# Kernel tuning notes

Measured on AMD Instinct MI355X. Metric: run time of the kernel, lower is better.

Reference implementation:

```python
import jax, jax.numpy as jnp
import numpy as np

# Decoder (keras) config: embed_dim=128, num_heads=8, num_att_layers=3, clip=10.0
B, NQ, NC, E, H, L, D = 512, 64, 1000, 128, 8, 3, 4
HD = E // H          # head_depth = 16
CLIP = 10.0


def setup_inputs() -> dict:
    key = jax.random.key(0)
    ks = jax.random.split(key, 12)
    s = 1.0 / np.sqrt(E)

    def w(k, shape):
        return jax.random.normal(k, shape, jnp.float32) * s

    return {
        "h": jax.random.normal(ks[0], (B, NQ, E), jnp.float32),
        "c": jax.random.normal(ks[1], (B, NC, E), jnp.float32),
        "mask": jnp.zeros((B, NQ, NC + 1), bool),
        "clusters": jnp.zeros((B, D, NC), bool),
        "depot_id": 0,
        # stacked per-layer GAT (multi-head self-attention) params [L, E, E]/[L, E]
        "gat_Wq": w(ks[2], (L, E, E)), "gat_bq": jnp.zeros((L, E), jnp.float32),
        "gat_Wk": w(ks[3], (L, E, E)), "gat_bk": jnp.zeros((L, E), jnp.float32),
        "gat_Wv": w(ks[4], (L, E, E)), "gat_bv": jnp.zeros((L, E), jnp.float32),
        "gat_Wo": w(ks[5], (L, E, E)), "gat_bo": jnp.zeros((L, E), jnp.float32),
        # decoder query/key dense layers (use_bias=True)
        "Wq": w(ks[6], (E, E)), "bq": jnp.zeros((E,), jnp.float32),
        "Wk": w(ks[7], (E, E)), "bk": jnp.zeros((E,), jnp.float32),
    }


def _mha_layer(x, Wq, bq, Wk, bk, Wv, bv, Wo, bo):
    # One Graph_Attention_Module: multi-head self-attention + residual.
    Bx, N, Ex = x.shape
    q = (x @ Wq + bq).reshape(Bx, N, H, HD)
    k = (x @ Wk + bk).reshape(Bx, N, H, HD)
    v = (x @ Wv + bv).reshape(Bx, N, H, HD)
    att = jax.nn.softmax(jnp.einsum('bqhd,bkhd->bhqk', q, k) / np.sqrt(HD), axis=-1)
    o = jnp.einsum('bhqk,bkhd->bqhd', att, v).reshape(Bx, N, Ex)
    return x + o @ Wo + bo


def reference(h, c, mask, clusters, depot_id,
              gat_Wq, gat_bq, gat_Wk, gat_bk, gat_Wv, gat_bv, gat_Wo, gat_bo,
              Wq, bq, Wk, bk):
    # --- MHGAT ---
    x = h
    for i in range(L):  # small fixed layer loop
        x = _mha_layer(x, gat_Wq[i], gat_bq[i], gat_Wk[i], gat_bk[i],
                       gat_Wv[i], gat_bv[i], gat_Wo[i], gat_bo[i])
    query = x @ Wq + bq            # [B, NQ, E]
    key = c @ Wk + bk              # [B, NC, E]
    # tanh-clipped compatibility: tanh(QK^T / sqrt(head_depth)) * clip
    compat = jnp.tanh(jnp.einsum('bqe,bke->bqk', query, key) / np.sqrt(HD)) * CLIP
    compat = jnp.where(mask[:, :, 1:], -jnp.inf, compat)   # drop depot column of mask

    # --- select_cust (vectorized: masked log_softmax + argmax per batch) ---
    compts = jnp.mean(compat, axis=1)          # [B, NC]
    clust = clusters[:, depot_id, :]           # [B, NC]
    tt = jnp.where(clust, -jnp.inf, compts)
    log_p = jax.nn.log_softmax(tt, axis=-1)
    action = jnp.argmax(log_p, axis=-1)[:, None]  # [B, 1]
    return action, compat
```

## Files before the change

### kernel.cpp

```cpp
#include <hip/hip_runtime.h>
#include <math.h>

#define NB   512
#define NQ   64
#define NCC  1000
#define EE   128
#define HH   8
#define HDD  16
#define NL   3
#define DD   4
#define KP   136
#define CCH  64
#define XP   136
#define VP   72

typedef __bf16 bf16x8 __attribute__((ext_vector_type(8)));
typedef unsigned short u16x8 __attribute__((ext_vector_type(8)));
typedef unsigned short u16x4 __attribute__((ext_vector_type(4)));
typedef unsigned int   u32x4 __attribute__((ext_vector_type(4)));
typedef float f32x4  __attribute__((ext_vector_type(4)));
typedef float f32x16 __attribute__((ext_vector_type(16)));

__device__ __forceinline__ unsigned short f2bf(float x) {
  union { float f; unsigned u; } v; v.f = x;
  unsigned r = (v.u + 0x7fffu + ((v.u >> 16) & 1u)) >> 16;
  return (unsigned short)r;
}
__device__ __forceinline__ float bf2f(unsigned short h) {
  union { unsigned u; float f; } v; v.u = ((unsigned)h) << 16;
  return v.f;
}
__device__ __forceinline__ bf16x8 ld8(const unsigned short* p) {
  return __builtin_bit_cast(bf16x8, *(const u16x8*)p);
}
__device__ __forceinline__ float tanh10_q(float s) {
  const float e = __expf(s * 0.5f);
  return 10.f - 20.f * __builtin_amdgcn_rcpf(e + 1.f);
}

__global__ __launch_bounds__(256) void wprep_kernel(
    const float* __restrict__ gWq, const float* __restrict__ gWk,
    const float* __restrict__ gWv, const float* __restrict__ gWo,
    const float* __restrict__ Wq,  const float* __restrict__ Wk,
    unsigned short* __restrict__ gwt_hi, unsigned short* __restrict__ gwt_lo)
{
  const int idx = blockIdx.x * 256 + threadIdx.x;
  const int m = idx >> 14;
  const int r = idx & 16383;
  const int k = r >> 7, n = r & 127;
  const float* src;
  if (m < 12) {
    const int l = m >> 2, w = m & 3;
    src = (w == 0 ? gWq : w == 1 ? gWk : w == 2 ? gWv : gWo) + l * 16384;
  } else if (m == 12) src = Wq;
  else                src = Wk;
  const float v = src[k * EE + n];
  const unsigned short h = f2bf(v);
  gwt_hi[(size_t)m * 16384 + n * EE + k] = h;
  gwt_lo[(size_t)m * 16384 + n * EE + k] = f2bf(v - bf2f(h));
}

__global__ __launch_bounds__(512, 1) void gat_query_mfma(
    const float* __restrict__ hin,
    const unsigned short* __restrict__ gwt_hi,
    const unsigned short* __restrict__ gwt_lo,
    const float* __restrict__ gbq, const float* __restrict__ gbk,
    const float* __restrict__ gbv, const float* __restrict__ gbo,
    const float* __restrict__ bq,
    float* __restrict__ query)
{
  __shared__ unsigned short XH[64 * XP], XL[64 * XP];
  __shared__ unsigned short QH[64 * XP], QL[64 * XP];
  __shared__ unsigned short KH[64 * XP], KL[64 * XP];
  __shared__ unsigned short VTH[128 * VP], VTL[128 * VP];

  const int b    = blockIdx.x;
  const int tid  = threadIdx.x;
  const int wid  = tid >> 6;
  const int lane = tid & 63;
  const int l15  = lane & 15;
  const int quad = lane >> 4;
  const int col  = lane & 31;
  const int hi32 = lane >> 5;

  for (int idx = tid; idx < NQ * EE; idx += 512) {
    const float v = hin[(size_t)b * NQ * EE + idx];
    const int r = idx >> 7, c = idx & 127;
    const unsigned short h = f2bf(v);
    XH[r * XP + c] = h;
    XL[r * XP + c] = f2bf(v - bf2f(h));
  }
  __syncthreads();

  const int mt = wid >> 1, nh = wid & 1;
  const int r0 = mt * 16;

  for (int l = 0; l < NL; ++l) {
    {
      bf16x8 axh[4], axl[4];
      #pragma unroll
      for (int k4 = 0; k4 < 4; ++k4) {
        axh[k4] = ld8(&XH[(r0 + l15) * XP + k4 * 32 + quad * 8]);
        axl[k4] = ld8(&XL[(r0 + l15) * XP + k4 * 32 + quad * 8]);
      }
      #pragma unroll
      for (int m = 0; m < 3; ++m) {
        const unsigned short* WH = gwt_hi + (size_t)(l * 4 + m) * 16384;
        const unsigned short* WL = gwt_lo + (size_t)(l * 4 + m) * 16384;
        const float* bias = (m == 0 ? gbq : (m == 1 ? gbk : gbv)) + l * EE;
        #pragma unroll
        for (int ntl = 0; ntl < 4; ++ntl) {
          const int n = (nh * 4 + ntl) * 16 + l15;
          f32x4 acc = (f32x4){0.f, 0.f, 0.f, 0.f};
          #pragma unroll
          for (int k4 = 0; k4 < 4; ++k4) {
            const int k0 = k4 * 32 + quad * 8;
            const bf16x8 bh = ld8(&WH[n * EE + k0]);
            const bf16x8 bl = ld8(&WL[n * EE + k0]);
            acc = __builtin_amdgcn_mfma_f32_16x16x32_bf16(axh[k4], bh, acc, 0, 0, 0);
            acc = __builtin_amdgcn_mfma_f32_16x16x32_bf16(axh[k4], bl, acc, 0, 0, 0);
            acc = __builtin_amdgcn_mfma_f32_16x16x32_bf16(axl[k4], bh, acc, 0, 0, 0);
          }
          const float bv = bias[n];
          if (m == 2) {
            u16x4 hv, lv;
            #pragma unroll
            for (int r = 0; r < 4; ++r) {
              const float v = acc[r] + bv;
              const unsigned short h = f2bf(v);
              hv[r] = h;
              lv[r] = f2bf(v - bf2f(h));
            }
            *(u16x4*)&VTH[n * VP + r0 + quad * 4] = hv;
            *(u16x4*)&VTL[n * VP + r0 + quad * 4] = lv;
          } else {
            unsigned short* DH = m ? KH : QH;
            unsigned short* DL = m ? KL : QL;
            #pragma unroll
            for (int r = 0; r < 4; ++r) {
              const int crow = r0 + quad * 4 + r;
              const float v = acc[r] + bv;
              const unsigned short h = f2bf(v);
              DH[crow * XP + n] = h;
              DL[crow * XP + n] = f2bf(v - bf2f(h));
            }
          }
        }
      }
    }
    __syncthreads();

    {
      const int hwid = wid;
      const int hb = hwid * 16 + hi32 * 8;
      bf16x8 akh[2], akl[2], qbh[2], qbl[2];
      #pragma unroll
      for (int t = 0; t < 2; ++t) {
        akh[t] = ld8(&KH[(t * 32 + col) * XP + hb]);
        akl[t] = ld8(&KL[(t * 32 + col) * XP + hb]);
        qbh[t] = ld8(&QH[(t * 32 + col) * XP + hb]);
        qbl[t] = ld8(&QL[(t * 32 + col) * XP + hb]);
      }

      bf16x8 pah[2][4], pal[2][4];
      #pragma unroll
      for (int qt = 0; qt < 2; ++qt) {
        f32x16 sAcc[2];
        #pragma unroll
        for (int kt = 0; kt < 2; ++kt) {
          #pragma unroll
          for (int i = 0; i < 16; ++i) sAcc[kt][i] = 0.f;
          sAcc[kt] = __builtin_amdgcn_mfma_f32_32x32x16_bf16(akh[kt], qbh[qt], sAcc[kt], 0, 0, 0);
          sAcc[kt] = __builtin_amdgcn_mfma_f32_32x32x16_bf16(akh[kt], qbl[qt], sAcc[kt], 0, 0, 0);
          sAcc[kt] = __builtin_amdgcn_mfma_f32_32x32x16_bf16(akl[kt], qbh[qt], sAcc[kt], 0, 0, 0);
        }
        float p[2][16];
        float mx = -INFINITY;
        #pragma unroll
        for (int kt = 0; kt < 2; ++kt)
          #pragma unroll
          for (int r = 0; r < 16; ++r) {
            p[kt][r] = sAcc[kt][r] * 0.25f;
            mx = fmaxf(mx, p[kt][r]);
          }
        mx = fmaxf(mx, __shfl_xor(mx, 32));
        float sum = 0.f;
        #pragma unroll
        for (int kt = 0; kt < 2; ++kt)
          #pragma unroll
          for (int r = 0; r < 16; ++r) {
            p[kt][r] = exp2f((p[kt][r] - mx) * 1.4426950408889634f);
            sum += p[kt][r];
          }
        sum += __shfl_xor(sum, 32);
        const float inv = 1.f / sum;

        unsigned pkh[2][8], pkl[2][8], swh[2][8], swl[2][8];
        #pragma unroll
        for (int kt = 0; kt < 2; ++kt)
          #pragma unroll
          for (int w = 0; w < 8; ++w) {
            const float v0 = p[kt][w * 2]     * inv;
            const float v1 = p[kt][w * 2 + 1] * inv;
            const unsigned short h0 = f2bf(v0);
            const unsigned short l0 = f2bf(v0 - bf2f(h0));
            const unsigned short h1 = f2bf(v1);
            const unsigned short l1 = f2bf(v1 - bf2f(h1));
            pkh[kt][w] = (unsigned)h0 | ((unsigned)h1 << 16);
            pkl[kt][w] = (unsigned)l0 | ((unsigned)l1 << 16);
            swh[kt][w] = (unsigned)__shfl_xor((int)pkh[kt][w], 32);
            swl[kt][w] = (unsigned)__shfl_xor((int)pkl[kt][w], 32);
          }
        const bool top = (hi32 != 0);
        #pragma unroll
        for (int ks = 0; ks < 4; ++ks) {
          const int kt = ks >> 1, hf = ks & 1;
          u32x4 wh, wl;
          wh[0] = top ? swh[kt][4 * hf + 2] : pkh[kt][4 * hf + 0];
          wh[1] = top ? swh[kt][4 * hf + 3] : pkh[kt][4 * hf + 1];
          wh[2] = top ? pkh[kt][4 * hf + 2] : swh[kt][4 * hf + 0];
          wh[3] = top ? pkh[kt][4 * hf + 3] : swh[kt][4 * hf + 1];
          wl[0] = top ? swl[kt][4 * hf + 2] : pkl[kt][4 * hf + 0];
          wl[1] = top ? swl[kt][4 * hf + 3] : pkl[kt][4 * hf + 1];
          wl[2] = top ? pkl[kt][4 * hf + 2] : swl[kt][4 * hf + 0];
          wl[3] = top ? pkl[kt][4 * hf + 3] : swl[kt][4 * hf + 1];
          pah[qt][ks] = __builtin_bit_cast(bf16x8, wh);
          pal[qt][ks] = __builtin_bit_cast(bf16x8, wl);
        }
      }

      bf16x8 bvh[4], bvl[4];
      const int vrow = hwid * 16 + (col & 15);
      #pragma unroll
      for (int ks = 0; ks < 4; ++ks) {
        bvh[ks] = ld8(&VTH[vrow * VP + ks * 16 + hi32 * 8]);
        bvl[ks] = ld8(&VTL[vrow * VP + ks * 16 + hi32 * 8]);
      }
      f32x16 accO[2];
      #pragma unroll
      for (int qt = 0; qt < 2; ++qt) {
        #pragma unroll
        for (int i = 0; i < 16; ++i) accO[qt][i] = 0.f;
        #pragma unroll
        for (int ks = 0; ks < 4; ++ks) {
          accO[qt] = __builtin_amdgcn_mfma_f32_32x32x16_bf16(pah[qt][ks], bvh[ks], accO[qt], 0, 0, 0);
          accO[qt] = __builtin_amdgcn_mfma_f32_32x32x16_bf16(pah[qt][ks], bvl[ks], accO[qt], 0, 0, 0);
          accO[qt] = __builtin_amdgcn_mfma_f32_32x32x16_bf16(pal[qt][ks], bvh[ks], accO[qt], 0, 0, 0);
        }
      }
      if (col < 16) {
        #pragma unroll
        for (int qt = 0; qt < 2; ++qt)
          #pragma unroll
          for (int r = 0; r < 16; ++r) {
            const int qrow = qt * 32 + (r & 3) + 8 * (r >> 2) + 4 * hi32;
            const float v = accO[qt][r];
            const unsigned short h = f2bf(v);
            KH[qrow * XP + hwid * 16 + col] = h;
            KL[qrow * XP + hwid * 16 + col] = f2bf(v - bf2f(h));
          }
      }
    }
    __syncthreads();

    {
      bf16x8 aoh[4], aol[4];
      #pragma unroll
      for (int k4 = 0; k4 < 4; ++k4) {
        aoh[k4] = ld8(&KH[(r0 + l15) * XP + k4 * 32 + quad * 8]);
        aol[k4] = ld8(&KL[(r0 + l15) * XP + k4 * 32 + quad * 8]);
      }
      const unsigned short* WH = gwt_hi + (size_t)(l * 4 + 3) * 16384;
      const unsigned short* WL = gwt_lo + (size_t)(l * 4 + 3) * 16384;
      #pragma unroll
      for (int ntl = 0; ntl < 4; ++ntl) {
        const int n = (nh * 4 + ntl) * 16 + l15;
        f32x4 acc = (f32x4){0.f, 0.f, 0.f, 0.f};
        #pragma unroll
        for (int k4 = 0; k4 < 4; ++k4) {
          const int k0 = k4 * 32 + quad * 8;
          const bf16x8 bh = ld8(&WH[n * EE + k0]);
          const bf16x8 bl = ld8(&WL[n * EE + k0]);
          acc = __builtin_amdgcn_mfma_f32_16x16x32_bf16(aoh[k4], bh, acc, 0, 0, 0);
          acc = __builtin_amdgcn_mfma_f32_16x16x32_bf16(aoh[k4], bl, acc, 0, 0, 0);
          acc = __builtin_amdgcn_mfma_f32_16x16x32_bf16(aol[k4], bh, acc, 0, 0, 0);
        }
        const float bv = gbo[l * EE + n];
        #pragma unroll
        for (int r = 0; r < 4; ++r) {
          const int crow = r0 + quad * 4 + r;
          const float xo = bf2f(XH[crow * XP + n]) + bf2f(XL[crow * XP + n]);
          const float v = xo + acc[r] + bv;
          const unsigned short h = f2bf(v);
          XH[crow * XP + n] = h;
          XL[crow * XP + n] = f2bf(v - bf2f(h));
        }
      }
    }
    __syncthreads();
  }

  {
    bf16x8 axh[4], axl[4];
    #pragma unroll
    for (int k4 = 0; k4 < 4; ++k4) {
      axh[k4] = ld8(&XH[(r0 + l15) * XP + k4 * 32 + quad * 8]);
      axl[k4] = ld8(&XL[(r0 + l15) * XP + k4 * 32 + quad * 8]);
    }
    const unsigned short* WH = gwt_hi + (size_t)12 * 16384;
    const unsigned short* WL = gwt_lo + (size_t)12 * 16384;
    #pragma unroll
    for (int ntl = 0; ntl < 4; ++ntl) {
      const int n = (nh * 4 + ntl) * 16 + l15;
      f32x4 acc = (f32x4){0.f, 0.f, 0.f, 0.f};
      #pragma unroll
      for (int k4 = 0; k4 < 4; ++k4) {
        const int k0 = k4 * 32 + quad * 8;
        const bf16x8 bh = ld8(&WH[n * EE + k0]);
        const bf16x8 bl = ld8(&WL[n * EE + k0]);
        acc = __builtin_amdgcn_mfma_f32_16x16x32_bf16(axh[k4], bh, acc, 0, 0, 0);
        acc = __builtin_amdgcn_mfma_f32_16x16x32_bf16(axh[k4], bl, acc, 0, 0, 0);
        acc = __builtin_amdgcn_mfma_f32_16x16x32_bf16(axl[k4], bh, acc, 0, 0, 0);
      }
      const float bv = bq[n];
      #pragma unroll
      for (int r = 0; r < 4; ++r) {
        const int crow = r0 + quad * 4 + r;
        query[((size_t)b * NQ + crow) * EE + n] = acc[r] + bv;
      }
    }
  }
}

__global__ __launch_bounds__(256, 4) void compat_mfma_kernel(
    const float* __restrict__ cin,
    const float* __restrict__ query,
    const unsigned char* __restrict__ mask,
    const unsigned short* __restrict__ wkt_hi,
    const unsigned short* __restrict__ wkt_lo,
    const float* __restrict__ bk,
    float* __restrict__ compat_out,
    float* __restrict__ compts)
{
  __shared__ unsigned short Khi[CCH * KP];
  __shared__ unsigned short Klo[CCH * KP];
  __shared__ float colsum[CCH];

  const int ch   = blockIdx.x;
  const int b    = blockIdx.y;
  const int tid  = threadIdx.x;
  const int wave = tid >> 6;
  const int lane = tid & 63;
  const int l15  = lane & 15;
  const int quad = lane >> 4;

  if (tid < CCH) colsum[tid] = 0.f;

  {
    float xv[4][8];
    {
      int grow = ch * CCH + wave * 16 + l15;
      if (grow > NCC - 1) grow = NCC - 1;
      const float* srow = &cin[((size_t)b * NCC + grow) * EE + quad * 8];
      #pragma unroll
      for (int k4 = 0; k4 < 4; ++k4) {
        *(float4*)&xv[k4][0] = *(const float4*)&srow[k4 * 32 + 0];
        *(float4*)&xv[k4][4] = *(const float4*)&srow[k4 * 32 + 4];
      }
    }
    bf16x8 ahi[4], alo[4];
    #pragma unroll
    for (int k4 = 0; k4 < 4; ++k4) {
      u16x8 h, lo;
      #pragma unroll
      for (int j = 0; j < 8; ++j) {
        unsigned short hb = f2bf(xv[k4][j]);
        h[j] = hb;
        lo[j] = f2bf(xv[k4][j] - bf2f(hb));
      }
      ahi[k4] = __builtin_bit_cast(bf16x8, h);
      alo[k4] = __builtin_bit_cast(bf16x8, lo);
    }

    #pragma unroll
    for (int nt = 0; nt < 8; ++nt) {
      const int n = nt * 16 + l15;
      f32x4 acc = (f32x4){0.f, 0.f, 0.f, 0.f};
      #pragma unroll
      for (int k4 = 0; k4 < 4; ++k4) {
        const int k0 = k4 * 32 + quad * 8;
        const bf16x8 bhi = __builtin_bit_cast(bf16x8, *(const u16x8*)&wkt_hi[n * EE + k0]);
        const bf16x8 blo = __builtin_bit_cast(bf16x8, *(const u16x8*)&wkt_lo[n * EE + k0]);
        acc = __builtin_amdgcn_mfma_f32_16x16x32_bf16(ahi[k4], bhi, acc, 0, 0, 0);
        acc = __builtin_amdgcn_mfma_f32_16x16x32_bf16(ahi[k4], blo, acc, 0, 0, 0);
        acc = __builtin_amdgcn_mfma_f32_16x16x32_bf16(alo[k4], bhi, acc, 0, 0, 0);
      }
      const float bkv = bk[n];
      #pragma unroll
      for (int r = 0; r < 4; ++r) {
        const int crow = wave * 16 + quad * 4 + r;
        const float v = acc[r] + bkv;
        const unsigned short hb = f2bf(v);
        Khi[crow * KP + n] = hb;
        Klo[crow * KP + n] = f2bf(v - bf2f(hb));
      }
    }
  }
  __syncthreads();

  {
    bf16x8 qhi[4], qlo[4];
    #pragma unroll
    for (int k4 = 0; k4 < 4; ++k4) {
      const float* src = &query[((size_t)b * NQ + wave * 16 + l15) * EE + k4 * 32 + quad * 8];
      const float4 x0 = *(const float4*)&src[0];
      const float4 x1 = *(const float4*)&src[4];
      float xq[8] = {x0.x, x0.y, x0.z, x0.w, x1.x, x1.y, x1.z, x1.w};
      u16x8 h, lo;
      #pragma unroll
      for (int j = 0; j < 8; ++j) {
        unsigned short hb = f2bf(xq[j]);
        h[j] = hb;
        lo[j] = f2bf(xq[j] - bf2f(hb));
      }
      qhi[k4] = __builtin_bit_cast(bf16x8, h);
      qlo[k4] = __builtin_bit_cast(bf16x8, lo);
    }

    f32x4 acc[4];
    #pragma unroll
    for (int nt = 0; nt < 4; ++nt) acc[nt] = (f32x4){0.f, 0.f, 0.f, 0.f};

    #pragma unroll
    for (int k4 = 0; k4 < 4; ++k4) {
      const int k0 = k4 * 32 + quad * 8;
      #pragma unroll
      for (int nt = 0; nt < 4; ++nt) {
        const int crow = nt * 16 + l15;
        const bf16x8 khf = __builtin_bit_cast(bf16x8, *(const u16x8*)&Khi[crow * KP + k0]);
        const bf16x8 klf = __builtin_bit_cast(bf16x8, *(const u16x8*)&Klo[crow * KP + k0]);
        acc[nt] = __builtin_amdgcn_mfma_f32_16x16x32_bf16(qhi[k4], khf, acc[nt], 0, 0, 0);
        acc[nt] = __builtin_amdgcn_mfma_f32_16x16x32_bf16(qhi[k4], klf, acc[nt], 0, 0, 0);
        acc[nt] = __builtin_amdgcn_mfma_f32_16x16x32_bf16(qlo[k4], khf, acc[nt], 0, 0, 0);
      }
    }

    #pragma unroll
    for (int nt = 0; nt < 4; ++nt) {
      const int jloc  = nt * 16 + l15;
      const int jglob = ch * CCH + jloc;
      const bool jok  = (jglob < NCC);
      float s4 = 0.f;
      #pragma unroll
      for (int r = 0; r < 4; ++r) {
        const int q = wave * 16 + quad * 4 + r;
        float v = tanh10_q(acc[nt][r]);
        if (jok) {
          if (mask[((size_t)b * NQ + q) * (NCC + 1) + 1 + jglob]) v = -INFINITY;
          compat_out[((size_t)b * NQ + q) * NCC + jglob] = v;
        }
        s4 += v;
      }
      s4 += __shfl_xor(s4, 16);
      s4 += __shfl_xor(s4, 32);
      if (lane < 16 && jok) atomicAdd(&colsum[jloc], s4);
    }
  }
  __syncthreads();

  if (tid < CCH) {
    const int jglob = ch * CCH + tid;
    if (jglob < NCC)
      compts[(size_t)b * 1024 + jglob] = colsum[tid] * (1.0f / (float)NQ);
  }
}

__global__ __launch_bounds__(256) void argmax_kernel(
    const float* __restrict__ compts,
    const unsigned char* __restrict__ clusters,
    const int* __restrict__ depot_id,
    float* __restrict__ out)
{
  __shared__ float redv[256];
  __shared__ int   redi[256];
  const int b   = blockIdx.x;
  const int tid = threadIdx.x;
  const int dep = depot_id[0];
  float bestv = -INFINITY;
  int   besti = 0x7fffffff;
  for (int j = tid; j < NCC; j += 256) {
    float t = compts[(size_t)b * 1024 + j];
    if (clusters[((size_t)b * DD + dep) * NCC + j]) t = -INFINITY;
    if (t > bestv || (t == bestv && j < besti)) { bestv = t; besti = j; }
  }
  redv[tid] = bestv; redi[tid] = besti;
  __syncthreads();
  if (tid == 0) {
    float bv = redv[0]; int bi = redi[0];
    for (int t = 1; t < 256; ++t) {
      if (redv[t] > bv || (redv[t] == bv && redi[t] < bi)) {
        bv = redv[t]; bi = redi[t];
      }
    }
    out[b] = (float)bi;
  }
}

extern "C" void kernel_launch(void* const* d_in, const int* in_sizes, int n_in,
                              void* d_out, int out_size, void* d_ws, size_t ws_size,
                              hipStream_t stream) {
  const float* hin      = (const float*)d_in[0];
  const float* cin      = (const float*)d_in[1];
  const unsigned char* mask     = (const unsigned char*)d_in[2];
  const unsigned char* clusters = (const unsigned char*)d_in[3];
  const int*   depot    = (const int*)d_in[4];
  const float* gWq = (const float*)d_in[5];
  const float* gbq = (const float*)d_in[6];
  const float* gWk = (const float*)d_in[7];
  const float* gbk = (const float*)d_in[8];
  const float* gWv = (const float*)d_in[9];
  const float* gbv = (const float*)d_in[10];
  const float* gWo = (const float*)d_in[11];
  const float* gbo = (const float*)d_in[12];
  const float* Wq  = (const float*)d_in[13];
  const float* bq  = (const float*)d_in[14];
  const float* Wk  = (const float*)d_in[15];
  const float* bk  = (const float*)d_in[16];
  float* out   = (float*)d_out;
  float* compat_out = out + NB;

  float*          query  = (float*)d_ws;
  float*          compts = (float*)((char*)d_ws + (size_t)NB * NQ * EE * 4);
  unsigned short* gwt_hi = (unsigned short*)((char*)compts + (size_t)NB * 1024 * 4);
  unsigned short* gwt_lo = gwt_hi + (size_t)14 * 16384;
  unsigned short* wkt_hi = gwt_hi + (size_t)13 * 16384;
  unsigned short* wkt_lo = gwt_lo + (size_t)13 * 16384;

  wprep_kernel<<<896, 256, 0, stream>>>(gWq, gWk, gWv, gWo, Wq, Wk, gwt_hi, gwt_lo);
  gat_query_mfma<<<NB, 512, 0, stream>>>(hin, gwt_hi, gwt_lo,
                                         gbq, gbk, gbv, gbo, bq, query);
  compat_mfma_kernel<<<dim3(16, NB), 256, 0, stream>>>(
      cin, query, mask, wkt_hi, wkt_lo, bk, compat_out, compts);
  argmax_kernel<<<NB, 256, 0, stream>>>(compts, clusters, depot, out);
}
```

Before: 959.9 us.

## Pre-split query and Wk into MFMA fragment layouts; stage c via swizzled LDS

The GAT kernel now splits the final query into bf16 hi/lo and writes it in MFMA fragment order, so the compat kernel loads ready-made operands instead of reloading fp32 and converting. Wk is also prearranged into fragment-ordered hi/lo tiles, giving fully coalesced contiguous weight loads. Input c is loaded with coalesced float4 reads into an XOR-swizzled LDS tile that is reused for the K results, which cuts strided global reads and bank conflicts. The cost is an extra LDS round trip and sync, plus a larger shared-memory footprint in the compat kernel.

```diff
diff --git a/kernel.cpp b/kernel.cpp
--- a/kernel.cpp
+++ b/kernel.cpp
@@ -9,7 +9,6 @@
 #define HDD  16
 #define NL   3
 #define DD   4
-#define KP   136
 #define CCH  64
 #define XP   136
 #define VP   72
@@ -37,12 +36,16 @@
   const float e = __expf(s * 0.5f);
   return 10.f - 20.f * __builtin_amdgcn_rcpf(e + 1.f);
 }
+__device__ __forceinline__ int swz(int row, int cb) {
+  return row * 256 + (cb ^ ((row & 7) << 4));
+}
 
 __global__ __launch_bounds__(256) void wprep_kernel(
     const float* __restrict__ gWq, const float* __restrict__ gWk,
     const float* __restrict__ gWv, const float* __restrict__ gWo,
     const float* __restrict__ Wq,  const float* __restrict__ Wk,
-    unsigned short* __restrict__ gwt_hi, unsigned short* __restrict__ gwt_lo)
+    unsigned short* __restrict__ gwt_hi, unsigned short* __restrict__ gwt_lo,
+    unsigned short* __restrict__ wkf_hi, unsigned short* __restrict__ wkf_lo)
 {
   const int idx = blockIdx.x * 256 + threadIdx.x;
   const int m = idx >> 14;
@@ -55,9 +58,18 @@
   } else if (m == 12) src = Wq;
   else                src = Wk;
   const float v = src[k * EE + n];
-  const unsigned short h = f2bf(v);
-  gwt_hi[(size_t)m * 16384 + n * EE + k] = h;
-  gwt_lo[(size_t)m * 16384 + n * EE + k] = f2bf(v - bf2f(h));
+  const unsigned short h  = f2bf(v);
+  const unsigned short lo = f2bf(v - bf2f(h));
+  if (m < 13) {
+    gwt_hi[(size_t)m * 16384 + n * EE + k] = h;
+    gwt_lo[(size_t)m * 16384 + n * EE + k] = lo;
+  } else {
+    const int nt = n >> 4, l15 = n & 15;
+    const int k4 = k >> 5, qd = (k >> 3) & 3, j = k & 7;
+    const int off = (((nt * 4 + k4) * 64) + qd * 16 + l15) * 8 + j;
+    wkf_hi[off] = h;
+    wkf_lo[off] = lo;
+  }
 }
 
 __global__ __launch_bounds__(512, 1) void gat_query_mfma(
@@ -67,7 +79,7 @@
     const float* __restrict__ gbq, const float* __restrict__ gbk,
     const float* __restrict__ gbv, const float* __restrict__ gbo,
     const float* __restrict__ bq,
-    float* __restrict__ query)
+    unsigned short* __restrict__ qhi, unsigned short* __restrict__ qlo)
 {
   __shared__ unsigned short XH[64 * XP], XL[64 * XP];
   __shared__ unsigned short QH[64 * XP], QL[64 * XP];
@@ -326,24 +338,44 @@
       #pragma unroll
       for (int r = 0; r < 4; ++r) {
         const int crow = r0 + quad * 4 + r;
-        query[((size_t)b * NQ + crow) * EE + n] = acc[r] + bv;
-      }
-    }
+        const float v = acc[r] + bv;
+        const unsigned short h = f2bf(v);
+        QH[crow * XP + n] = h;
+        QL[crow * XP + n] = f2bf(v - bf2f(h));
+      }
+    }
+  }
+  __syncthreads();
+
+  for (int it = 0; it < 4; ++it) {
+    const int idx  = it * 512 + tid;
+    const int part = idx >> 10;
+    const int id2  = idx & 1023;
+    const int wc   = id2 >> 8;
+    const int k4   = (id2 >> 6) & 3;
+    const int ln   = id2 & 63;
+    const int row  = wc * 16 + (ln & 15);
+    const int colu = k4 * 32 + (ln >> 4) * 8;
+    const unsigned short* S = part ? QL : QH;
+    const u16x8 v = *(const u16x8*)&S[row * XP + colu];
+    unsigned short* D = part ? qlo : qhi;
+    *(u16x8*)&D[((((size_t)b * 4 + wc) * 4 + k4) * 64 + ln) * 8] = v;
   }
 }
 
 __global__ __launch_bounds__(256, 4) void compat_mfma_kernel(
     const float* __restrict__ cin,
-    const float* __restrict__ query,
+    const unsigned short* __restrict__ qhi,
+    const unsigned short* __restrict__ qlo,
     const unsigned char* __restrict__ mask,
-    const unsigned short* __restrict__ wkt_hi,
-    const unsigned short* __restrict__ wkt_lo,
+    const unsigned short* __restrict__ wkf_hi,
+    const unsigned short* __restrict__ wkf_lo,
     const float* __restrict__ bk,
     float* __restrict__ compat_out,
     float* __restrict__ compts)
 {
-  __shared__ unsigned short Khi[CCH * KP];
-  __shared__ unsigned short Klo[CCH * KP];
+  __shared__ unsigned short TH[64 * 128];
+  __shared__ unsigned short TL[64 * 128];
   __shared__ float colsum[CCH];
 
   const int ch   = blockIdx.x;
@@ -356,44 +388,49 @@
 
   if (tid < CCH) colsum[tid] = 0.f;
 
+  #pragma unroll
+  for (int it = 0; it < 8; ++it) {
+    const int lin = it * 256 + tid;
+    const int row = lin >> 5;
+    const int c16 = lin & 31;
+    int grow = ch * CCH + row;
+    if (grow > NCC - 1) grow = NCC - 1;
+    const float4 x = *(const float4*)&cin[((size_t)b * NCC + grow) * EE + c16 * 4];
+    const float xv[4] = {x.x, x.y, x.z, x.w};
+    u16x4 h, l;
+    #pragma unroll
+    for (int j = 0; j < 4; ++j) {
+      const unsigned short hb = f2bf(xv[j]);
+      h[j] = hb;
+      l[j] = f2bf(xv[j] - bf2f(hb));
+    }
+    const int byt = swz(row, c16 * 8);
+    *(u16x4*)((char*)TH + byt) = h;
+    *(u16x4*)((char*)TL + byt) = l;
+  }
+  __syncthreads();
+
   {
-    float xv[4][8];
-    {
-      int grow = ch * CCH + wave * 16 + l15;
-      if (grow > NCC - 1) grow = NCC - 1;
-      const float* srow = &cin[((size_t)b * NCC + grow) * EE + quad * 8];
-      #pragma unroll
-      for (int k4 = 0; k4 < 4; ++k4) {
-        *(float4*)&xv[k4][0] = *(const float4*)&srow[k4 * 32 + 0];
-        *(float4*)&xv[k4][4] = *(const float4*)&srow[k4 * 32 + 4];
-      }
-    }
     bf16x8 ahi[4], alo[4];
+    const int arow = wave * 16 + l15;
     #pragma unroll
     for (int k4 = 0; k4 < 4; ++k4) {
-      u16x8 h, lo;
-      #pragma unroll
-      for (int j = 0; j < 8; ++j) {
-        unsigned short hb = f2bf(xv[k4][j]);
-        h[j] = hb;
-        lo[j] = f2bf(xv[k4][j] - bf2f(hb));
-      }
-      ahi[k4] = __builtin_bit_cast(bf16x8, h);
-      alo[k4] = __builtin_bit_cast(bf16x8, lo);
-    }
-
+      const int byt = swz(arow, k4 * 64 + quad * 16);
+      ahi[k4] = *(const bf16x8*)((char*)TH + byt);
+      alo[k4] = *(const bf16x8*)((char*)TL + byt);
+    }
     #pragma unroll
     for (int nt = 0; nt < 8; ++nt) {
       const int n = nt * 16 + l15;
       f32x4 acc = (f32x4){0.f, 0.f, 0.f, 0.f};
       #pragma unroll
       for (int k4 = 0; k4 < 4; ++k4) {
-        const int k0 = k4 * 32 + quad * 8;
-        const bf16x8 bhi = __builtin_bit_cast(bf16x8, *(const u16x8*)&wkt_hi[n * EE + k0]);
-        const bf16x8 blo = __builtin_bit_cast(bf16x8, *(const u16x8*)&wkt_lo[n * EE + k0]);
-        acc = __builtin_amdgcn_mfma_f32_16x16x32_bf16(ahi[k4], bhi, acc, 0, 0, 0);
-        acc = __builtin_amdgcn_mfma_f32_16x16x32_bf16(ahi[k4], blo, acc, 0, 0, 0);
-        acc = __builtin_amdgcn_mfma_f32_16x16x32_bf16(alo[k4], bhi, acc, 0, 0, 0);
+        const size_t foff = (size_t)((nt * 4 + k4) * 64 + lane) * 8;
+        const bf16x8 bh = ld8(&wkf_hi[foff]);
+        const bf16x8 bl = ld8(&wkf_lo[foff]);
+        acc = __builtin_amdgcn_mfma_f32_16x16x32_bf16(ahi[k4], bh, acc, 0, 0, 0);
+        acc = __builtin_amdgcn_mfma_f32_16x16x32_bf16(ahi[k4], bl, acc, 0, 0, 0);
+        acc = __builtin_amdgcn_mfma_f32_16x16x32_bf16(alo[k4], bh, acc, 0, 0, 0);
       }
       const float bkv = bk[n];
       #pragma unroll
@@ -401,30 +438,21 @@
         const int crow = wave * 16 + quad * 4 + r;
         const float v = acc[r] + bkv;
         const unsigned short hb = f2bf(v);
-        Khi[crow * KP + n] = hb;
-        Klo[crow * KP + n] = f2bf(v - bf2f(hb));
+        const int byt = swz(crow, n * 2);
+        *(unsigned short*)((char*)TH + byt) = hb;
+        *(unsigned short*)((char*)TL + byt) = f2bf(v - bf2f(hb));
       }
     }
   }
   __syncthreads();
 
   {
-    bf16x8 qhi[4], qlo[4];
+    bf16x8 qh[4], ql[4];
     #pragma unroll
     for (int k4 = 0; k4 < 4; ++k4) {
-      const float* src = &query[((size_t)b * NQ + wave * 16 + l15) * EE + k4 * 32 + quad * 8];
-      const float4 x0 = *(const float4*)&src[0];
-      const float4 x1 = *(const float4*)&src[4];
-      float xq[8] = {x0.x, x0.y, x0.z, x0.w, x1.x, x1.y, x1.z, x1.w};
-      u16x8 h, lo;
-      #pragma unroll
-      for (int j = 0; j < 8; ++j) {
-        unsigned short hb = f2bf(xq[j]);
-        h[j] = hb;
-        lo[j] = f2bf(xq[j] - bf2f(hb));
-      }
-      qhi[k4] = __builtin_bit_cast(bf16x8, h);
-      qlo[k4] = __builtin_bit_cast(bf16x8, lo);
+      const size_t qoff = ((((size_t)b * 4 + wave) * 4 + k4) * 64 + lane) * 8;
+      qh[k4] = ld8(&qhi[qoff]);
+      ql[k4] = ld8(&qlo[qoff]);
     }
 
     f32x4 acc[4];
@@ -433,15 +461,15 @@
 
     #pragma unroll
     for (int k4 = 0; k4 < 4; ++k4) {
-      const int k0 = k4 * 32 + quad * 8;
       #pragma unroll
       for (int nt = 0; nt < 4; ++nt) {
-        const int crow = nt * 16 + l15;
-        const bf16x8 khf = __builtin_bit_cast(bf16x8, *(const u16x8*)&Khi[crow * KP + k0]);
-        const bf16x8 klf = __builtin_bit_cast(bf16x8, *(const u16x8*)&Klo[crow * KP + k0]);
-        acc[nt] = __builtin_amdgcn_mfma_f32_16x16x32_bf16(qhi[k4], khf, acc[nt], 0, 0, 0);
-        acc[nt] = __builtin_amdgcn_mfma_f32_16x16x32_bf16(qhi[k4], klf, acc[nt], 0, 0, 0);
-        acc[nt] = __builtin_amdgcn_mfma_f32_16x16x32_bf16(qlo[k4], khf, acc[nt], 0, 0, 0);
+        const int krow = nt * 16 + l15;
+        const int byt = swz(krow, k4 * 64 + quad * 16);
+        const bf16x8 khf = *(const bf16x8*)((char*)TH + byt);
+        const bf16x8 klf = *(const bf16x8*)((char*)TL + byt);
+        acc[nt] = __builtin_amdgcn_mfma_f32_16x16x32_bf16(qh[k4], khf, acc[nt], 0, 0, 0);
+        acc[nt] = __builtin_amdgcn_mfma_f32_16x16x32_bf16(qh[k4], klf, acc[nt], 0, 0, 0);
+        acc[nt] = __builtin_amdgcn_mfma_f32_16x16x32_bf16(ql[k4], khf, acc[nt], 0, 0, 0);
       }
     }
 
@@ -529,17 +557,19 @@
   float* out   = (float*)d_out;
   float* compat_out = out + NB;
 
-  float*          query  = (float*)d_ws;
-  float*          compts = (float*)((char*)d_ws + (size_t)NB * NQ * EE * 4);
+  unsigned short* qhi    = (unsigned short*)d_ws;
+  unsigned short* qlo    = qhi + (size_t)NB * 4 * 4 * 64 * 8;
+  float*          compts = (float*)(qlo + (size_t)NB * 4 * 4 * 64 * 8);
   unsigned short* gwt_hi = (unsigned short*)((char*)compts + (size_t)NB * 1024 * 4);
   unsigned short* gwt_lo = gwt_hi + (size_t)14 * 16384;
-  unsigned short* wkt_hi = gwt_hi + (size_t)13 * 16384;
-  unsigned short* wkt_lo = gwt_lo + (size_t)13 * 16384;
-
-  wprep_kernel<<<896, 256, 0, stream>>>(gWq, gWk, gWv, gWo, Wq, Wk, gwt_hi, gwt_lo);
+  unsigned short* wkf_hi = gwt_lo + (size_t)14 * 16384;
+  unsigned short* wkf_lo = wkf_hi + (size_t)16384;
+
+  wprep_kernel<<<896, 256, 0, stream>>>(gWq, gWk, gWv, gWo, Wq, Wk,
+                                        gwt_hi, gwt_lo, wkf_hi, wkf_lo);
   gat_query_mfma<<<NB, 512, 0, stream>>>(hin, gwt_hi, gwt_lo,
-                                         gbq, gbk, gbv, gbo, bq, query);
+                                         gbq, gbk, gbv, gbo, bq, qhi, qlo);
   compat_mfma_kernel<<<dim3(16, NB), 256, 0, stream>>>(
-      cin, query, mask, wkt_hi, wkt_lo, bk, compat_out, compts);
+      cin, qhi, qlo, mask, wkf_hi, wkf_lo, bk, compat_out, compts);
   argmax_kernel<<<NB, 256, 0, stream>>>(compts, clusters, depot, out);
 }
```

After: 828.5 us. -13.7%, faster.
